# Performance work log

Hardware: AMD Instinct MI355X
Metric: run time of the kernel (lower is better)

## Reference

```python
import jax, jax.numpy as jnp
import numpy as np

# ---- model / data constants ----
B, N, D, L = 32, 96, 64, 5          # graphs, nodes per graph, hidden, layers
EP = 768                             # directed edges per graph (symmetrized in to_dense)
NODE_VOCAB = 11                      # matches LocalFWL2(..., 11, 5, 'instance')
EDGE_VOCAB = 5                       # edge labels 0..4; index 5 = 'no edge' embedding row
EPS = 1e-5


def setup_inputs() -> dict:
    key = jax.random.key(0)
    ks = jax.random.split(key, 12)
    # block-contiguous batch: graph b owns nodes [b*N, (b+1)*N)
    x = jax.random.randint(ks[0], (B * N,), 0, NODE_VOCAB)
    u = jax.random.randint(ks[1], (B, EP), 0, N)
    v = jax.random.randint(ks[2], (B, EP), 0, N)
    off = (jnp.arange(B) * N)[:, None]
    edge_index = jnp.stack([(u + off).reshape(-1), (v + off).reshape(-1)], axis=0)
    edge_attr = jax.random.randint(ks[3], (B * EP,), 0, EDGE_VOCAB)
    s = 0.1
    inv = 1.0 / np.sqrt(D)
    return {
        "x": x,
        "edge_index": edge_index,
        "edge_attr": edge_attr,
        "node_emb": jax.random.normal(ks[4], (NODE_VOCAB, D), jnp.float32) * s,
        "edge_emb": jax.random.normal(ks[5], (EDGE_VOCAB + 1, D), jnp.float32) * s,
        "W1": jax.random.normal(ks[6], (L, D, D), jnp.float32) * inv,
        "b1": jnp.zeros((L, D), jnp.float32),
        "W2": jax.random.normal(ks[7], (L, D, D), jnp.float32) * inv,
        "b2": jnp.zeros((L, D), jnp.float32),
        "Wm": jax.random.normal(ks[8], (L, D, D), jnp.float32) * inv,
        "bm": jnp.zeros((L, D), jnp.float32),
        "gamma": jnp.ones((L, D), jnp.float32),
        "beta": jnp.zeros((L, D), jnp.float32),
        "pool_w": jax.random.normal(ks[9], (D, 1), jnp.float32) * inv,
        "pool_b": jnp.zeros((1,), jnp.float32),
    }


def reference(x, edge_index, edge_attr, node_emb, edge_emb,
              W1, b1, W2, b2, Wm, bm, gamma, beta, pool_w, pool_b):
    # ---- to_dense: sparse edge list -> dense per-graph edge-label matrix ----
    g = edge_index[0] // N
    u = edge_index[0] % N
    v = edge_index[1] % N
    A = jnp.full((B, N, N), EDGE_VOCAB, dtype=jnp.int32)        # EDGE_VOCAB = no-edge
    ea = edge_attr.astype(jnp.int32)
    A = A.at[g, u, v].set(ea)
    A = A.at[g, v, u].set(ea)                                    # undirected
    adj = (A != EDGE_VOCAB).astype(node_emb.dtype)               # [B,N,N]

    # ---- pair-state init: W_uv = h_u + h_v + edge_emb(A_uv) ----
    H = node_emb[x.reshape(B, N)]                                # [B,N,D]
    W = H[:, :, None, :] + H[:, None, :, :] + edge_emb[A]        # [B,N,N,D]

    # ---- local FWL(2) layers ----
    for l in range(L):
        h1 = jax.nn.relu(jnp.einsum('buwd,de->buwe', W, W1[l]) + b1[l])
        h2 = jax.nn.relu(jnp.einsum('bwvd,de->bwve', W, W2[l]) + b2[l])
        # aggregate over w restricted to neighbors of v (local FWL2)
        M = jnp.einsum('buwd,bwv,bwvd->buvd', h1, adj, h2)       # [B,N,N,D]
        W = W + jnp.einsum('buvd,de->buve', M, Wm[l]) + bm[l]
        # instance norm over the pair dims (u,v), per graph, per channel
        mu = W.mean(axis=(1, 2), keepdims=True)
        var = W.var(axis=(1, 2), keepdims=True)
        W = gamma[l] * (W - mu) * jax.lax.rsqrt(var + EPS) + beta[l]
        W = jax.nn.relu(W)

    # ---- pooling: sum over all pairs, then Linear(D, 1), squeeze ----
    pooled = W.sum(axis=(1, 2))                                  # [B,D]
    return (pooled @ pool_w + pool_b).squeeze(-1)                # [B]
```

## Files before the change

### kernel.cpp

```cpp
#include <hip/hip_runtime.h>
#include <hip/hip_bf16.h>

#define B_ 32
#define N_ 96
#define D_ 64
#define L_ 5
#define BE_ 24576
#define NN_ 9216
#define BNN_ 294912
#define EPS_ 1e-5f
#define INV_NN (1.0f/9216.0f)

typedef unsigned short u16;
typedef unsigned int u32;
typedef __attribute__((ext_vector_type(8))) short bf16x8;
typedef __attribute__((ext_vector_type(4))) float f32x4;

__device__ __forceinline__ float bf2f(u16 r){ return __uint_as_float(((u32)r) << 16); }
__device__ __forceinline__ u32 f2bf(float f){
  u32 u = __float_as_uint(f);
  return (u + 0x7fffu + ((u >> 16) & 1u)) >> 16;
}
__device__ __forceinline__ u32 pack2(float lo, float hi){
  return f2bf(lo) | (f2bf(hi) << 16);
}

__global__ void k_scatter(const int* __restrict__ ei, const int* __restrict__ ea,
                          int* __restrict__ A)
{
  int e = blockIdx.x * 256 + threadIdx.x;
  if (e >= BE_) return;
  int a = ei[e], bnode = ei[BE_ + e];
  int g = a / N_;
  int u = a % N_;
  int v = bnode % N_;
  int lab = ea[e] & 7;
  int base = g * NN_;
  atomicMax(&A[base + u * N_ + v], ((e + 1) << 3) | lab);
  atomicMax(&A[base + v * N_ + u], ((BE_ + e + 1) << 3) | lab);
}

__launch_bounds__(256)
__global__ void k_winit(const int* __restrict__ x, const int* __restrict__ A,
                        const float* __restrict__ nemb, const float* __restrict__ eemb,
                        u16* __restrict__ W)
{
  int gid = blockIdx.x * 256 + threadIdx.x;
  int d = (gid & 31) * 2;
  int p = gid >> 5;
  int b = p / NN_;
  int rem = p % NN_;
  int u = rem / N_;
  int v = rem % N_;
  int xu = x[b * N_ + u], xv = x[b * N_ + v];
  int pk = A[p];
  int lab = pk ? (pk & 7) : 5;
  float v0 = nemb[xu * 64 + d]     + nemb[xv * 64 + d]     + eemb[lab * 64 + d];
  float v1 = nemb[xu * 64 + d + 1] + nemb[xv * 64 + d + 1] + eemb[lab * 64 + d + 1];
  ((u32*)W)[gid] = pack2(v0, v1);
}

__global__ void k_prep(const float* __restrict__ W1, const float* __restrict__ W2,
                       const float* __restrict__ Wm, u16* __restrict__ WT)
{
  int idx = blockIdx.x * 256 + threadIdx.x;
  if (idx >= 15 * 4096) return;
  int l3 = idx >> 12;
  int r  = idx & 4095;
  int e = r >> 6, d = r & 63;
  int l = l3 / 3, which = l3 % 3;
  const float* s = which == 0 ? W1 : which == 1 ? W2 : Wm;
  WT[idx] = (u16)f2bf(s[l * 4096 + d * 64 + e]);
}

__launch_bounds__(256)
__global__ void k_lin2(const u16* __restrict__ W, const u16* __restrict__ WT1,
                       const u16* __restrict__ WT2,
                       const float* __restrict__ b1l, const float* __restrict__ b2l,
                       const int* __restrict__ A,
                       const float* __restrict__ stp, const float* __restrict__ gml,
                       const float* __restrict__ btl,
                       int use_norm, u16* __restrict__ h1, u16* __restrict__ g2)
{
  __shared__ u16 Cs[64 * 264];
  const int tid = threadIdx.x;
  const int wave = tid >> 6, lane = tid & 63;
  const int lm = lane & 15, lg = lane >> 4;
  const int b = blockIdx.x / 36;
  const int qbase = (blockIdx.x % 36) * 256;

  float sc[2][8], sh[2][8];
  if (use_norm) {
    #pragma unroll
    for (int s = 0; s < 2; ++s) {
      int d0 = s * 32 + lg * 8;
      #pragma unroll
      for (int j = 0; j < 8; j += 2) {
        float4 t = *(const float4*)(stp + ((size_t)b * 64 + d0 + j) * 2);
        float2 g = *(const float2*)(gml + d0 + j);
        float2 bb = *(const float2*)(btl + d0 + j);
        float mu0 = t.x * INV_NN;
        float var0 = fmaf(t.y, INV_NN, -mu0 * mu0);
        float s0 = g.x * rsqrtf(var0 + EPS_);
        sc[s][j] = s0;
        sh[s][j] = fmaf(-mu0, s0, bb.x);
        float mu1 = t.z * INV_NN;
        float var1 = fmaf(t.w, INV_NN, -mu1 * mu1);
        float s1v = g.y * rsqrtf(var1 + EPS_);
        sc[s][j + 1] = s1v;
        sh[s][j + 1] = fmaf(-mu1, s1v, bb.y);
      }
    }
  } else {
    #pragma unroll
    for (int s = 0; s < 2; ++s)
      #pragma unroll
      for (int j = 0; j < 8; ++j) { sc[s][j] = 1.f; sh[s][j] = 0.f; }
  }

  bf16x8 bF[4][2];
  int flags[4];
  #pragma unroll
  for (int qt = 0; qt < 4; ++qt) {
    int q = qbase + wave * 64 + qt * 16 + lm;
    const u16* wrow = W + ((size_t)b * NN_ + q) * 64;
    flags[qt] = A[b * NN_ + q];
    #pragma unroll
    for (int s = 0; s < 2; ++s) {
      bf16x8 raw = *(const bf16x8*)(wrow + s * 32 + lg * 8);
      if (use_norm) {
        bf16x8 bb;
        #pragma unroll
        for (int j = 0; j < 8; ++j) {
          float v = bf2f((u16)raw[j]);
          v = fmaxf(fmaf(v, sc[s][j], sh[s][j]), 0.f);
          bb[j] = (short)f2bf(v);
        }
        bF[qt][s] = bb;
      } else {
        bF[qt][s] = raw;
      }
    }
  }

  const f32x4 zf = {0.f, 0.f, 0.f, 0.f};

  {
    bf16x8 aF[4][2];
    #pragma unroll
    for (int et = 0; et < 4; ++et)
      #pragma unroll
      for (int s = 0; s < 2; ++s)
        aF[et][s] = *(const bf16x8*)(WT1 + (et * 16 + lm) * 64 + s * 32 + lg * 8);
    f32x4 acc[4][4];
    #pragma unroll
    for (int i = 0; i < 4; ++i)
      #pragma unroll
      for (int j = 0; j < 4; ++j) acc[i][j] = zf;
    #pragma unroll
    for (int qt = 0; qt < 4; ++qt)
      #pragma unroll
      for (int s = 0; s < 2; ++s)
        #pragma unroll
        for (int et = 0; et < 4; ++et)
          acc[qt][et] = __builtin_amdgcn_mfma_f32_16x16x32_bf16(aF[et][s], bF[qt][s], acc[qt][et], 0, 0, 0);
    #pragma unroll
    for (int et = 0; et < 4; ++et) {
      float4 bs = *(const float4*)(b1l + et * 16 + lg * 4);
      float bv[4] = {bs.x, bs.y, bs.z, bs.w};
      #pragma unroll
      for (int qt = 0; qt < 4; ++qt) {
        int col = wave * 64 + qt * 16 + lm;
        #pragma unroll
        for (int r = 0; r < 4; ++r)
          Cs[(et * 16 + lg * 4 + r) * 264 + col] = (u16)f2bf(fmaxf(acc[qt][et][r] + bv[r], 0.f));
      }
    }
  }
  __syncthreads();
  {
    u16* ob = h1 + (size_t)b * 64 * NN_ + qbase;
    for (int i = tid; i < 2048; i += 256) {
      int e = i >> 5, qc = (i & 31) * 8;
      uint4 val = *(const uint4*)&Cs[e * 264 + qc];
      *(uint4*)(ob + (size_t)e * NN_ + qc) = val;
    }
  }
  __syncthreads();

  {
    bf16x8 aF[4][2];
    #pragma unroll
    for (int et = 0; et < 4; ++et)
      #pragma unroll
      for (int s = 0; s < 2; ++s)
        aF[et][s] = *(const bf16x8*)(WT2 + (et * 16 + lm) * 64 + s * 32 + lg * 8);
    f32x4 acc[4][4];
    #pragma unroll
    for (int i = 0; i < 4; ++i)
      #pragma unroll
      for (int j = 0; j < 4; ++j) acc[i][j] = zf;
    #pragma unroll
    for (int qt = 0; qt < 4; ++qt)
      #pragma unroll
      for (int s = 0; s < 2; ++s)
        #pragma unroll
        for (int et = 0; et < 4; ++et)
          acc[qt][et] = __builtin_amdgcn_mfma_f32_16x16x32_bf16(aF[et][s], bF[qt][s], acc[qt][et], 0, 0, 0);
    #pragma unroll
    for (int et = 0; et < 4; ++et) {
      float4 bs = *(const float4*)(b2l + et * 16 + lg * 4);
      float bv[4] = {bs.x, bs.y, bs.z, bs.w};
      #pragma unroll
      for (int qt = 0; qt < 4; ++qt) {
        int col = wave * 64 + qt * 16 + lm;
        #pragma unroll
        for (int r = 0; r < 4; ++r) {
          float v = fmaxf(acc[qt][et][r] + bv[r], 0.f);
          if (!flags[qt]) v = 0.f;
          Cs[(et * 16 + lg * 4 + r) * 264 + col] = (u16)f2bf(v);
        }
      }
    }
  }
  __syncthreads();
  {
    u16* ob = g2 + (size_t)b * 64 * NN_ + qbase;
    for (int i = tid; i < 2048; i += 256) {
      int e = i >> 5, qc = (i & 31) * 8;
      uint4 val = *(const uint4*)&Cs[e * 264 + qc];
      *(uint4*)(ob + (size_t)e * NN_ + qc) = val;
    }
  }
}

__launch_bounds__(256)
__global__ void k_einsum(const u16* __restrict__ h1, const u16* __restrict__ g2n,
                         u16* __restrict__ M)
{
  __shared__ u32 Bt[96 * 60];
  u16* Cst = (u16*)Bt;
  const int tid = threadIdx.x;
  const int wave = tid >> 6, lane = tid & 63;
  const int lm = lane & 15, lg = lane >> 4;
  const int bd = blockIdx.x;
  const u16* h1p = h1 + (size_t)bd * NN_;
  const u16* g2p = g2n + (size_t)bd * NN_;
  const int u0 = (wave & 1) * 48, v0 = (wave >> 1) * 48;

  #pragma unroll
  for (int it = 0; it < 9; ++it) {
    int p = it * 256 + tid;
    int wp = p / 48, vh = (p % 48) * 2;
    u32 a = *(const u32*)(g2p + (2 * wp) * 96 + vh);
    u32 c = *(const u32*)(g2p + (2 * wp + 1) * 96 + vh);
    Bt[vh * 60 + wp]       = (a & 0xffffu) | (c << 16);
    Bt[(vh + 1) * 60 + wp] = (a >> 16) | (c & 0xffff0000u);
  }

  bf16x8 aF[3][3];
  #pragma unroll
  for (int t = 0; t < 3; ++t)
    #pragma unroll
    for (int s = 0; s < 3; ++s)
      aF[t][s] = *(const bf16x8*)(h1p + (u0 + t * 16 + lm) * 96 + s * 32 + lg * 8);
  __syncthreads();

  bf16x8 bF[3][3];
  #pragma unroll
  for (int vt = 0; vt < 3; ++vt)
    #pragma unroll
    for (int s = 0; s < 3; ++s)
      bF[vt][s] = *(const bf16x8*)&Bt[(v0 + vt * 16 + lm) * 60 + s * 16 + lg * 4];
  __syncthreads();

  const f32x4 zf = {0.f, 0.f, 0.f, 0.f};
  f32x4 acc[3][3];
  #pragma unroll
  for (int i = 0; i < 3; ++i)
    #pragma unroll
    for (int j = 0; j < 3; ++j) acc[i][j] = zf;
  #pragma unroll
  for (int s = 0; s < 3; ++s)
    #pragma unroll
    for (int ut = 0; ut < 3; ++ut)
      #pragma unroll
      for (int vt = 0; vt < 3; ++vt)
        acc[ut][vt] = __builtin_amdgcn_mfma_f32_16x16x32_bf16(aF[ut][s], bF[vt][s], acc[ut][vt], 0, 0, 0);

  #pragma unroll
  for (int ut = 0; ut < 3; ++ut)
    #pragma unroll
    for (int vt = 0; vt < 3; ++vt)
      #pragma unroll
      for (int r = 0; r < 4; ++r)
        Cst[(u0 + ut * 16 + lg * 4 + r) * 104 + v0 + vt * 16 + lm] = (u16)f2bf(acc[ut][vt][r]);
  __syncthreads();
  u16* Mp = M + (size_t)bd * NN_;
  for (int i = tid; i < 1152; i += 256) {
    int u = i / 12, vc = (i % 12) * 8;
    uint4 val = *(const uint4*)&Cst[u * 104 + vc];
    *(uint4*)(Mp + u * 96 + vc) = val;
  }
}

__launch_bounds__(256)
__global__ void k_update(const u16* __restrict__ M, const u16* __restrict__ WmT,
                         const float* __restrict__ bml, u16* __restrict__ W,
                         const float* __restrict__ stp, const float* __restrict__ gml,
                         const float* __restrict__ btl, int use_norm,
                         float* __restrict__ sto)
{
  __shared__ u16 Mt[128 * 64];
  __shared__ float red[128];
  const int tid = threadIdx.x;
  const int wave = tid >> 6, lane = tid & 63;
  const int lm = lane & 15, lg = lane >> 4;
  const int b = blockIdx.x / 72;
  const int qblk = (blockIdx.x % 72) * 128;

  if (tid < 128) red[tid] = 0.f;

  bf16x8 aF[4][2];
  #pragma unroll
  for (int et = 0; et < 4; ++et)
    #pragma unroll
    for (int s = 0; s < 2; ++s)
      aF[et][s] = *(const bf16x8*)(WmT + (et * 16 + lm) * 64 + s * 32 + lg * 8);

  {
    const int dpl = tid >> 2;
    const int qob = tid & 3;
    const u16* Mb = M + (size_t)(b * 64 + dpl) * NN_ + qblk;
    #pragma unroll
    for (int t = 0; t < 4; ++t) {
      int qo = qob + t * 4;
      uint4 v = *(const uint4*)(Mb + qo * 8);
      u32 ws[4] = {v.x, v.y, v.z, v.w};
      #pragma unroll
      for (int h = 0; h < 4; ++h) {
        int j0 = h * 2;
        int q0 = qo * 8 + j0;
        int slot0 = (dpl >> 3) ^ j0 ^ (qo & 7);
        int slot1 = (dpl >> 3) ^ (j0 + 1) ^ (qo & 7);
        Mt[q0 * 64 + slot0 * 8 + (dpl & 7)]       = (u16)(ws[h] & 0xffffu);
        Mt[(q0 + 1) * 64 + slot1 * 8 + (dpl & 7)] = (u16)(ws[h] >> 16);
      }
    }
  }
  __syncthreads();

  const f32x4 zf = {0.f, 0.f, 0.f, 0.f};
  f32x4 acc[2][4];
  #pragma unroll
  for (int i = 0; i < 2; ++i)
    #pragma unroll
    for (int j = 0; j < 4; ++j) acc[i][j] = zf;

  #pragma unroll
  for (int qtL = 0; qtL < 2; ++qtL) {
    int ql = (wave * 2 + qtL) * 16 + lm;
    bf16x8 bF[2];
    #pragma unroll
    for (int s = 0; s < 2; ++s) {
      int slot = (s * 4 + lg) ^ (ql & 7) ^ ((ql >> 3) & 7);
      bF[s] = *(const bf16x8*)&Mt[ql * 64 + slot * 8];
    }
    #pragma unroll
    for (int s = 0; s < 2; ++s)
      #pragma unroll
      for (int et = 0; et < 4; ++et)
        acc[qtL][et] = __builtin_amdgcn_mfma_f32_16x16x32_bf16(aF[et][s], bF[s], acc[qtL][et], 0, 0, 0);
  }

  float s1[4][4], s2[4][4];
  #pragma unroll
  for (int i = 0; i < 4; ++i)
    #pragma unroll
    for (int j = 0; j < 4; ++j) { s1[i][j] = 0.f; s2[i][j] = 0.f; }

  #pragma unroll
  for (int et = 0; et < 4; ++et) {
    int e0 = et * 16 + lg * 4;
    float4 bs = *(const float4*)(bml + e0);
    float bv[4] = {bs.x, bs.y, bs.z, bs.w};
    float scn[4], shn[4];
    if (use_norm) {
      float4 t0 = *(const float4*)(stp + ((size_t)b * 64 + e0) * 2);
      float4 t1 = *(const float4*)(stp + ((size_t)b * 64 + e0) * 2 + 4);
      float4 gv = *(const float4*)(gml + e0);
      float4 bv2 = *(const float4*)(btl + e0);
      float S1v[4] = {t0.x, t0.z, t1.x, t1.z};
      float S2v[4] = {t0.y, t0.w, t1.y, t1.w};
      float gvv[4] = {gv.x, gv.y, gv.z, gv.w};
      float btv[4] = {bv2.x, bv2.y, bv2.z, bv2.w};
      #pragma unroll
      for (int r = 0; r < 4; ++r) {
        float mu = S1v[r] * INV_NN;
        float var = fmaf(S2v[r], INV_NN, -mu * mu);
        float s0 = gvv[r] * rsqrtf(var + EPS_);
        scn[r] = s0;
        shn[r] = fmaf(-mu, s0, btv[r]);
      }
    } else {
      #pragma unroll
      for (int r = 0; r < 4; ++r) { scn[r] = 1.f; shn[r] = 0.f; }
    }
    #pragma unroll
    for (int qtL = 0; qtL < 2; ++qtL) {
      int qg = qblk + (wave * 2 + qtL) * 16 + lm;
      u16* Wp = W + ((size_t)b * NN_ + qg) * 64 + e0;
      uint2 wo = *(const uint2*)Wp;
      float wv[4] = {bf2f((u16)(wo.x & 0xffff)), bf2f((u16)(wo.x >> 16)),
                     bf2f((u16)(wo.y & 0xffff)), bf2f((u16)(wo.y >> 16))};
      float o[4];
      #pragma unroll
      for (int r = 0; r < 4; ++r) {
        float res = use_norm ? fmaxf(fmaf(wv[r], scn[r], shn[r]), 0.f) : wv[r];
        float val = acc[qtL][et][r] + bv[r] + res;
        o[r] = val;
        s1[et][r] += val;
        s2[et][r] = fmaf(val, val, s2[et][r]);
      }
      uint2 ov;
      ov.x = pack2(o[0], o[1]);
      ov.y = pack2(o[2], o[3]);
      *(uint2*)Wp = ov;
    }
  }

  #pragma unroll
  for (int et = 0; et < 4; ++et)
    #pragma unroll
    for (int r = 0; r < 4; ++r) {
      float a = s1[et][r], c = s2[et][r];
      a += __shfl_xor(a, 1, 64); a += __shfl_xor(a, 2, 64);
      a += __shfl_xor(a, 4, 64); a += __shfl_xor(a, 8, 64);
      c += __shfl_xor(c, 1, 64); c += __shfl_xor(c, 2, 64);
      c += __shfl_xor(c, 4, 64); c += __shfl_xor(c, 8, 64);
      if (lm == 0) {
        int e = et * 16 + lg * 4 + r;
        atomicAdd(&red[e], a);
        atomicAdd(&red[64 + e], c);
      }
    }
  __syncthreads();
  if (tid < 64) atomicAdd(&sto[((size_t)b * 64 + tid) * 2], red[tid]);
  else if (tid < 128) atomicAdd(&sto[((size_t)b * 64 + (tid - 64)) * 2 + 1], red[tid]);
}

__launch_bounds__(256)
__global__ void k_pool(const u16* __restrict__ W,
                       const float* __restrict__ st,
                       const float* __restrict__ gml, const float* __restrict__ btl,
                       const float* __restrict__ pw, const float* __restrict__ pb,
                       float* __restrict__ out)
{
  const int b = blockIdx.x / 24;
  const int chunk = blockIdx.x % 24;
  const int tid = threadIdx.x;
  const int e = tid & 63;
  float S1 = st[(b * 64 + e) * 2], S2 = st[(b * 64 + e) * 2 + 1];
  float mu = S1 * INV_NN;
  float var = fmaf(S2, INV_NN, -mu * mu);
  float rsig = rsqrtf(var + EPS_);
  float scl = gml[e] * rsig;
  float shf = fmaf(-mu, scl, btl[e]);
  float pwv = pw[e];
  const u16* base = W + (size_t)b * NN_ * 64 + chunk * 24576;
  float s = 0.f;
  for (int k = 0; k < 96; k++) {
    float w = bf2f(base[k * 256 + tid]);
    s += fmaxf(fmaf(w, scl, shf), 0.f) * pwv;
  }
  for (int o = 32; o; o >>= 1) s += __shfl_down(s, o, 64);
  __shared__ float rs[4];
  if ((tid & 63) == 0) rs[tid >> 6] = s;
  __syncthreads();
  if (tid == 0) {
    float t = rs[0] + rs[1] + rs[2] + rs[3];
    if (chunk == 0) t += pb[0];
    atomicAdd(&out[b], t);
  }
}

extern "C" void kernel_launch(void* const* d_in, const int* in_sizes, int n_in,
                              void* d_out, int out_size, void* d_ws, size_t ws_size,
                              hipStream_t stream) {
  const int*   x    = (const int*)d_in[0];
  const int*   ei   = (const int*)d_in[1];
  const int*   ea   = (const int*)d_in[2];
  const float* nemb = (const float*)d_in[3];
  const float* eemb = (const float*)d_in[4];
  const float* W1   = (const float*)d_in[5];
  const float* b1   = (const float*)d_in[6];
  const float* W2   = (const float*)d_in[7];
  const float* b2   = (const float*)d_in[8];
  const float* Wm   = (const float*)d_in[9];
  const float* bm   = (const float*)d_in[10];
  const float* gm   = (const float*)d_in[11];
  const float* bt   = (const float*)d_in[12];
  const float* pw   = (const float*)d_in[13];
  const float* pb   = (const float*)d_in[14];

  char* ws = (char*)d_ws;
  const size_t OFF_A  = 0;
  const size_t OFF_W  = 1179648;
  const size_t OFF_H1 = 38928384;
  const size_t OFF_G2 = 76677120;
  const size_t OFF_M  = 114425856;
  const size_t OFF_ST = 152174592;
  const size_t OFF_WT = 152256512;
  const size_t NEED   = OFF_WT + 122880;
  if (ws_size < NEED) return;

  int*   A     = (int*)(ws + OFF_A);
  u16*   W     = (u16*)(ws + OFF_W);
  u16*   h1    = (u16*)(ws + OFF_H1);
  u16*   g2n   = (u16*)(ws + OFF_G2);
  u16*   M     = (u16*)(ws + OFF_M);
  float* stats = (float*)(ws + OFF_ST);
  u16*   WT    = (u16*)(ws + OFF_WT);
  float* out   = (float*)d_out;

  hipMemsetAsync(A, 0, 1179648, stream);
  hipMemsetAsync(stats, 0, 81920, stream);
  hipMemsetAsync(out, 0, 32 * sizeof(float), stream);

  k_prep<<<240, 256, 0, stream>>>(W1, W2, Wm, WT);
  k_scatter<<<96, 256, 0, stream>>>(ei, ea, A);
  k_winit<<<36864, 256, 0, stream>>>(x, A, nemb, eemb, W);

  for (int l = 0; l < L_; l++) {
    int un = (l > 0);
    const float* stp = un ? stats + (size_t)(l - 1) * 4096 : stats;
    const float* gml = un ? gm + (l - 1) * 64 : gm;
    const float* btl = un ? bt + (l - 1) * 64 : bt;
    float* sto = stats + (size_t)l * 4096;
    k_lin2<<<1152, 256, 0, stream>>>(W, WT + (l * 3 + 0) * 4096, WT + (l * 3 + 1) * 4096,
                                     b1 + l * 64, b2 + l * 64, A, stp, gml, btl, un, h1, g2n);
    k_einsum<<<2048, 256, 0, stream>>>(h1, g2n, M);
    k_update<<<2304, 256, 0, stream>>>(M, WT + (l * 3 + 2) * 4096, bm + l * 64, W,
                                       stp, gml, btl, un, sto);
  }
  k_pool<<<768, 256, 0, stream>>>(W, stats + 4 * 4096, gm + 4 * 64, bt + 4 * 64,
                                  pw, pb, out);
}
```

Measured before the change: 615.3 us.

## Replace atomic norm statistics with per-block partials and halve update block size

Instance-norm statistics are no longer accumulated with shared and global atomics. Each k_update block now writes its own partial sums to a buffer, and k_lin2 and k_pool reduce those partials. k_lin2 also writes the finished per-graph scale and shift into a small buffer that k_update reads, which removes the rsqrt work from k_update. k_update now runs 128-thread blocks over 64 pairs and prefetches the residual W rows earlier, and k_winit is vectorised to float4 loads. The trade is some repeated partial-sum reduction in each k_lin2 block and a larger workspace.

```diff
diff --git a/kernel.cpp b/kernel.cpp
--- a/kernel.cpp
+++ b/kernel.cpp
@@ -46,8 +46,8 @@
                         u16* __restrict__ W)
 {
   int gid = blockIdx.x * 256 + threadIdx.x;
-  int d = (gid & 31) * 2;
-  int p = gid >> 5;
+  int d = (gid & 15) * 4;
+  int p = gid >> 4;
   int b = p / NN_;
   int rem = p % NN_;
   int u = rem / N_;
@@ -55,9 +55,13 @@
   int xu = x[b * N_ + u], xv = x[b * N_ + v];
   int pk = A[p];
   int lab = pk ? (pk & 7) : 5;
-  float v0 = nemb[xu * 64 + d]     + nemb[xv * 64 + d]     + eemb[lab * 64 + d];
-  float v1 = nemb[xu * 64 + d + 1] + nemb[xv * 64 + d + 1] + eemb[lab * 64 + d + 1];
-  ((u32*)W)[gid] = pack2(v0, v1);
+  float4 nu = *(const float4*)(nemb + xu * 64 + d);
+  float4 nv = *(const float4*)(nemb + xv * 64 + d);
+  float4 ee = *(const float4*)(eemb + lab * 64 + d);
+  uint2 o;
+  o.x = pack2(nu.x + nv.x + ee.x, nu.y + nv.y + ee.y);
+  o.y = pack2(nu.z + nv.z + ee.z, nu.w + nv.w + ee.w);
+  ((uint2*)W)[gid] = o;
 }
 
 __global__ void k_prep(const float* __restrict__ W1, const float* __restrict__ W2,
@@ -78,38 +82,56 @@
                        const u16* __restrict__ WT2,
                        const float* __restrict__ b1l, const float* __restrict__ b2l,
                        const int* __restrict__ A,
-                       const float* __restrict__ stp, const float* __restrict__ gml,
-                       const float* __restrict__ btl,
+                       const float* __restrict__ pst, const float* __restrict__ gml,
+                       const float* __restrict__ btl, float* __restrict__ nsF,
                        int use_norm, u16* __restrict__ h1, u16* __restrict__ g2)
 {
   __shared__ u16 Cs[64 * 264];
+  __shared__ float nsS[128];
   const int tid = threadIdx.x;
   const int wave = tid >> 6, lane = tid & 63;
   const int lm = lane & 15, lg = lane >> 4;
   const int b = blockIdx.x / 36;
   const int qbase = (blockIdx.x % 36) * 256;
 
+  if (use_norm) {
+    if (tid < 128) {
+      const float* p = pst + ((size_t)b * 144) * 128 + tid;
+      float a0 = 0.f, a1 = 0.f, a2 = 0.f, a3 = 0.f;
+      for (int i = 0; i < 144; i += 4) {
+        a0 += p[(size_t)i * 128];
+        a1 += p[(size_t)(i + 1) * 128];
+        a2 += p[(size_t)(i + 2) * 128];
+        a3 += p[(size_t)(i + 3) * 128];
+      }
+      nsS[tid] = (a0 + a1) + (a2 + a3);
+    }
+    __syncthreads();
+  }
+
   float sc[2][8], sh[2][8];
   if (use_norm) {
     #pragma unroll
     for (int s = 0; s < 2; ++s) {
       int d0 = s * 32 + lg * 8;
       #pragma unroll
-      for (int j = 0; j < 8; j += 2) {
-        float4 t = *(const float4*)(stp + ((size_t)b * 64 + d0 + j) * 2);
-        float2 g = *(const float2*)(gml + d0 + j);
-        float2 bb = *(const float2*)(btl + d0 + j);
-        float mu0 = t.x * INV_NN;
-        float var0 = fmaf(t.y, INV_NN, -mu0 * mu0);
-        float s0 = g.x * rsqrtf(var0 + EPS_);
+      for (int j = 0; j < 8; ++j) {
+        int d = d0 + j;
+        float S1 = nsS[d], S2 = nsS[64 + d];
+        float mu = S1 * INV_NN;
+        float var = fmaf(S2, INV_NN, -mu * mu);
+        float s0 = gml[d] * rsqrtf(var + EPS_);
         sc[s][j] = s0;
-        sh[s][j] = fmaf(-mu0, s0, bb.x);
-        float mu1 = t.z * INV_NN;
-        float var1 = fmaf(t.w, INV_NN, -mu1 * mu1);
-        float s1v = g.y * rsqrtf(var1 + EPS_);
-        sc[s][j + 1] = s1v;
-        sh[s][j + 1] = fmaf(-mu1, s1v, bb.y);
-      }
+        sh[s][j] = fmaf(-mu, s0, btl[d]);
+      }
+    }
+    if ((blockIdx.x % 36) == 0 && tid < 64) {
+      float S1 = nsS[tid], S2 = nsS[64 + tid];
+      float mu = S1 * INV_NN;
+      float var = fmaf(S2, INV_NN, -mu * mu);
+      float s0 = gml[tid] * rsqrtf(var + EPS_);
+      nsF[((size_t)b * 64 + tid) * 2]     = s0;
+      nsF[((size_t)b * 64 + tid) * 2 + 1] = fmaf(-mu, s0, btl[tid]);
     }
   } else {
     #pragma unroll
@@ -304,22 +326,20 @@
   }
 }
 
-__launch_bounds__(256)
+__launch_bounds__(128)
 __global__ void k_update(const u16* __restrict__ M, const u16* __restrict__ WmT,
                          const float* __restrict__ bml, u16* __restrict__ W,
-                         const float* __restrict__ stp, const float* __restrict__ gml,
-                         const float* __restrict__ btl, int use_norm,
-                         float* __restrict__ sto)
-{
-  __shared__ u16 Mt[128 * 64];
-  __shared__ float red[128];
+                         const float* __restrict__ nsF, int use_norm,
+                         float* __restrict__ pst)
+{
+  __shared__ u16 Mt[64 * 64];
+  __shared__ float red[2][128];
   const int tid = threadIdx.x;
   const int wave = tid >> 6, lane = tid & 63;
   const int lm = lane & 15, lg = lane >> 4;
-  const int b = blockIdx.x / 72;
-  const int qblk = (blockIdx.x % 72) * 128;
-
-  if (tid < 128) red[tid] = 0.f;
+  const int b = blockIdx.x / 144;
+  const int qi = blockIdx.x % 144;
+  const int qblk = qi * 64;
 
   bf16x8 aF[4][2];
   #pragma unroll
@@ -328,13 +348,40 @@
     for (int s = 0; s < 2; ++s)
       aF[et][s] = *(const bf16x8*)(WmT + (et * 16 + lm) * 64 + s * 32 + lg * 8);
 
+  uint2 wres[2][4];
+  #pragma unroll
+  for (int qtL = 0; qtL < 2; ++qtL) {
+    int qg = qblk + (wave * 2 + qtL) * 16 + lm;
+    const u16* Wp = W + ((size_t)b * NN_ + qg) * 64;
+    #pragma unroll
+    for (int et = 0; et < 4; ++et)
+      wres[qtL][et] = *(const uint2*)(Wp + et * 16 + lg * 4);
+  }
+
+  float scn[4][4], shn[4][4];
+  if (use_norm) {
+    #pragma unroll
+    for (int et = 0; et < 4; ++et) {
+      int e0 = et * 16 + lg * 4;
+      float4 t0 = *(const float4*)(nsF + ((size_t)b * 64 + e0) * 2);
+      float4 t1 = *(const float4*)(nsF + ((size_t)b * 64 + e0) * 2 + 4);
+      scn[et][0] = t0.x; shn[et][0] = t0.y; scn[et][1] = t0.z; shn[et][1] = t0.w;
+      scn[et][2] = t1.x; shn[et][2] = t1.y; scn[et][3] = t1.z; shn[et][3] = t1.w;
+    }
+  } else {
+    #pragma unroll
+    for (int et = 0; et < 4; ++et)
+      #pragma unroll
+      for (int r = 0; r < 4; ++r) { scn[et][r] = 1.f; shn[et][r] = 0.f; }
+  }
+
   {
-    const int dpl = tid >> 2;
-    const int qob = tid & 3;
+    const int dpl = tid >> 1;
+    const int qob = tid & 1;
     const u16* Mb = M + (size_t)(b * 64 + dpl) * NN_ + qblk;
     #pragma unroll
     for (int t = 0; t < 4; ++t) {
-      int qo = qob + t * 4;
+      int qo = qob + t * 2;
       uint4 v = *(const uint4*)(Mb + qo * 8);
       u32 ws[4] = {v.x, v.y, v.z, v.w};
       #pragma unroll
@@ -384,39 +431,17 @@
     int e0 = et * 16 + lg * 4;
     float4 bs = *(const float4*)(bml + e0);
     float bv[4] = {bs.x, bs.y, bs.z, bs.w};
-    float scn[4], shn[4];
-    if (use_norm) {
-      float4 t0 = *(const float4*)(stp + ((size_t)b * 64 + e0) * 2);
-      float4 t1 = *(const float4*)(stp + ((size_t)b * 64 + e0) * 2 + 4);
-      float4 gv = *(const float4*)(gml + e0);
-      float4 bv2 = *(const float4*)(btl + e0);
-      float S1v[4] = {t0.x, t0.z, t1.x, t1.z};
-      float S2v[4] = {t0.y, t0.w, t1.y, t1.w};
-      float gvv[4] = {gv.x, gv.y, gv.z, gv.w};
-      float btv[4] = {bv2.x, bv2.y, bv2.z, bv2.w};
-      #pragma unroll
-      for (int r = 0; r < 4; ++r) {
-        float mu = S1v[r] * INV_NN;
-        float var = fmaf(S2v[r], INV_NN, -mu * mu);
-        float s0 = gvv[r] * rsqrtf(var + EPS_);
-        scn[r] = s0;
-        shn[r] = fmaf(-mu, s0, btv[r]);
-      }
-    } else {
-      #pragma unroll
-      for (int r = 0; r < 4; ++r) { scn[r] = 1.f; shn[r] = 0.f; }
-    }
     #pragma unroll
     for (int qtL = 0; qtL < 2; ++qtL) {
       int qg = qblk + (wave * 2 + qtL) * 16 + lm;
       u16* Wp = W + ((size_t)b * NN_ + qg) * 64 + e0;
-      uint2 wo = *(const uint2*)Wp;
+      uint2 wo = wres[qtL][et];
       float wv[4] = {bf2f((u16)(wo.x & 0xffff)), bf2f((u16)(wo.x >> 16)),
                      bf2f((u16)(wo.y & 0xffff)), bf2f((u16)(wo.y >> 16))};
       float o[4];
       #pragma unroll
       for (int r = 0; r < 4; ++r) {
-        float res = use_norm ? fmaxf(fmaf(wv[r], scn[r], shn[r]), 0.f) : wv[r];
+        float res = use_norm ? fmaxf(fmaf(wv[r], scn[et][r], shn[et][r]), 0.f) : wv[r];
         float val = acc[qtL][et][r] + bv[r] + res;
         o[r] = val;
         s1[et][r] += val;
@@ -440,27 +465,40 @@
       c += __shfl_xor(c, 4, 64); c += __shfl_xor(c, 8, 64);
       if (lm == 0) {
         int e = et * 16 + lg * 4 + r;
-        atomicAdd(&red[e], a);
-        atomicAdd(&red[64 + e], c);
-      }
-    }
-  __syncthreads();
-  if (tid < 64) atomicAdd(&sto[((size_t)b * 64 + tid) * 2], red[tid]);
-  else if (tid < 128) atomicAdd(&sto[((size_t)b * 64 + (tid - 64)) * 2 + 1], red[tid]);
+        red[wave][e]      = a;
+        red[wave][64 + e] = c;
+      }
+    }
+  __syncthreads();
+  if (tid < 128)
+    pst[((size_t)b * 144 + qi) * 128 + tid] = red[0][tid] + red[1][tid];
 }
 
 __launch_bounds__(256)
 __global__ void k_pool(const u16* __restrict__ W,
-                       const float* __restrict__ st,
+                       const float* __restrict__ pst,
                        const float* __restrict__ gml, const float* __restrict__ btl,
                        const float* __restrict__ pw, const float* __restrict__ pb,
                        float* __restrict__ out)
 {
+  __shared__ float nsS[128];
   const int b = blockIdx.x / 24;
   const int chunk = blockIdx.x % 24;
   const int tid = threadIdx.x;
+  if (tid < 128) {
+    const float* p = pst + ((size_t)b * 144) * 128 + tid;
+    float a0 = 0.f, a1 = 0.f, a2 = 0.f, a3 = 0.f;
+    for (int i = 0; i < 144; i += 4) {
+      a0 += p[(size_t)i * 128];
+      a1 += p[(size_t)(i + 1) * 128];
+      a2 += p[(size_t)(i + 2) * 128];
+      a3 += p[(size_t)(i + 3) * 128];
+    }
+    nsS[tid] = (a0 + a1) + (a2 + a3);
+  }
+  __syncthreads();
   const int e = tid & 63;
-  float S1 = st[(b * 64 + e) * 2], S2 = st[(b * 64 + e) * 2 + 1];
+  float S1 = nsS[e], S2 = nsS[64 + e];
   float mu = S1 * INV_NN;
   float var = fmaf(S2, INV_NN, -mu * mu);
   float rsig = rsqrtf(var + EPS_);
@@ -509,8 +547,9 @@
   const size_t OFF_H1 = 38928384;
   const size_t OFF_G2 = 76677120;
   const size_t OFF_M  = 114425856;
-  const size_t OFF_ST = 152174592;
-  const size_t OFF_WT = 152256512;
+  const size_t OFF_PS = 152174592;
+  const size_t OFF_NF = 154533888;
+  const size_t OFF_WT = 154550272;
   const size_t NEED   = OFF_WT + 122880;
   if (ws_size < NEED) return;
 
@@ -519,30 +558,28 @@
   u16*   h1    = (u16*)(ws + OFF_H1);
   u16*   g2n   = (u16*)(ws + OFF_G2);
   u16*   M     = (u16*)(ws + OFF_M);
-  float* stats = (float*)(ws + OFF_ST);
+  float* pst   = (float*)(ws + OFF_PS);
+  float* nsF   = (float*)(ws + OFF_NF);
   u16*   WT    = (u16*)(ws + OFF_WT);
   float* out   = (float*)d_out;
 
   hipMemsetAsync(A, 0, 1179648, stream);
-  hipMemsetAsync(stats, 0, 81920, stream);
   hipMemsetAsync(out, 0, 32 * sizeof(float), stream);
 
   k_prep<<<240, 256, 0, stream>>>(W1, W2, Wm, WT);
   k_scatter<<<96, 256, 0, stream>>>(ei, ea, A);
-  k_winit<<<36864, 256, 0, stream>>>(x, A, nemb, eemb, W);
+  k_winit<<<18432, 256, 0, stream>>>(x, A, nemb, eemb, W);
 
   for (int l = 0; l < L_; l++) {
     int un = (l > 0);
-    const float* stp = un ? stats + (size_t)(l - 1) * 4096 : stats;
     const float* gml = un ? gm + (l - 1) * 64 : gm;
     const float* btl = un ? bt + (l - 1) * 64 : bt;
-    float* sto = stats + (size_t)l * 4096;
     k_lin2<<<1152, 256, 0, stream>>>(W, WT + (l * 3 + 0) * 4096, WT + (l * 3 + 1) * 4096,
-                                     b1 + l * 64, b2 + l * 64, A, stp, gml, btl, un, h1, g2n);
+                                     b1 + l * 64, b2 + l * 64, A, pst, gml, btl, nsF,
+                                     un, h1, g2n);
     k_einsum<<<2048, 256, 0, stream>>>(h1, g2n, M);
-    k_update<<<2304, 256, 0, stream>>>(M, WT + (l * 3 + 2) * 4096, bm + l * 64, W,
-                                       stp, gml, btl, un, sto);
-  }
-  k_pool<<<768, 256, 0, stream>>>(W, stats + 4 * 4096, gm + 4 * 64, bt + 4 * 64,
-                                  pw, pb, out);
-}
+    k_update<<<4608, 128, 0, stream>>>(M, WT + (l * 3 + 2) * 4096, bm + l * 64, W,
+                                       nsF, un, pst);
+  }
+  k_pool<<<768, 256, 0, stream>>>(W, pst, gm + 4 * 64, bt + 4 * 64, pw, pb, out);
+}
```

Result: faster. 581.2 us (-5.5%).
